# Optimization experiments

Measured on AMD Instinct MI355X. Metric: run time of the kernel, lower is better.

## Reference

```python
import jax, jax.numpy as jnp
import numpy as np

EMB = 512
N_MODELS = 5
HID = 64
N_Q = 2048
N_P = 256


def setup_inputs() -> dict:
    key = jax.random.key(0)
    ks = jax.random.split(key, 6)
    return {
        "query_features": jax.random.normal(ks[0], (N_Q, EMB), dtype=jnp.float32),
        "prototypes": jax.random.normal(ks[1], (N_P, EMB), dtype=jnp.float32),
        # first Linear: weight [64, 2*EMB], bias [64], per model
        "W1": jax.random.normal(ks[2], (N_MODELS, HID, 2 * EMB), dtype=jnp.float32) * 0.02,
        "b1": jax.random.normal(ks[3], (N_MODELS, HID), dtype=jnp.float32) * 0.02,
        # second Linear: weight [1, 64] -> stored as [64], bias scalar per model
        "W2": jax.random.normal(ks[4], (N_MODELS, HID), dtype=jnp.float32) * 0.02,
        "b2": jax.random.normal(ks[5], (N_MODELS,), dtype=jnp.float32) * 0.02,
    }


def reference(query_features, prototypes, W1, b1, W2, b2):
    d = query_features.shape[1]
    # cat([q_i, p_j]) @ W1^T == q_i @ W1[:, :d]^T + p_j @ W1[:, d:]^T
    W1q = W1[:, :, :d]   # [M, H, d]
    W1p = W1[:, :, d:]   # [M, H, d]
    hq = jnp.einsum('qd,mhd->mqh', query_features, W1q)  # [M, Q, H]
    hp = jnp.einsum('pd,mhd->mph', prototypes, W1p)      # [M, P, H]
    h = jax.nn.relu(hq[:, :, None, :] + hp[:, None, :, :] + b1[:, None, None, :])  # [M, Q, P, H]
    out = jnp.einsum('mqph,mh->mqp', h, W2) + b2[:, None, None]  # [M, Q, P]
    mean_d = out.mean(axis=0)
    # torch.std default is unbiased (ddof=1)
    unc = jnp.std(out, axis=0, ddof=1)
    return mean_d * jnp.exp(-unc)
```

## Files before the change

### kernel.cpp

```cpp
#include <hip/hip_runtime.h>
#include <math.h>

#define EMB 512
#define NM 5
#define HID 64
#define NQ 2048
#define NP 256
#define NROWS 2304
#define NRT 144
#define NC 16

typedef __attribute__((ext_vector_type(8))) short short8;
typedef __attribute__((ext_vector_type(4))) float floatx4;

#define A_BY      0u
#define B_BY      2621440u
#define PXH_BY    2949120u
#define PXL_BY    5308416u
#define PWH_BY    7667712u
#define PWL_BY    8323072u

__device__ inline unsigned short bfr(float f) {
    unsigned u = __float_as_uint(f);
    u += 0x7FFFu + ((u >> 16) & 1u);
    return (unsigned short)(u >> 16);
}

__global__ __launch_bounds__(256) void conv_pack(const float* __restrict__ Q,
                                                 const float* __restrict__ P,
                                                 const float* __restrict__ W1,
                                                 char* __restrict__ ws) {
    short* PXH = (short*)(ws + PXH_BY);
    short* PXL = (short*)(ws + PXL_BY);
    short* PWH = (short*)(ws + PWH_BY);
    short* PWL = (short*)(ws + PWL_BY);

    int lane = threadIdx.x & 63;
    int wid  = blockIdx.x * 4 + (threadIdx.x >> 6);
    int kq   = (lane >> 4) * 8;

    const float* src;
    short *dh, *dl;
    if (wid < NRT * NC) {
        int rt = wid >> 4, c = wid & 15;
        int r  = rt * 16 + (lane & 15);
        src = (r < NQ ? Q + (size_t)r * EMB : P + (size_t)(r - NQ) * EMB)
              + c * 32 + kq;
        dh = PXH + (size_t)wid * 512 + lane * 8;
        dl = PXL + (size_t)wid * 512 + lane * 8;
    } else {
        int u = wid - NRT * NC;
        int c = u & 15, ht = (u >> 4) & 3, half = (u >> 6) & 1, m = u >> 7;
        int h = ht * 16 + (lane & 15);
        src = W1 + ((size_t)m * 64 + h) * 1024 + half * EMB + c * 32 + kq;
        dh = PWH + (size_t)u * 512 + lane * 8;
        dl = PWL + (size_t)u * 512 + lane * 8;
    }

    float4 v0 = *(const float4*)&src[0];
    float4 v1 = *(const float4*)&src[4];
    short8 hh, ll;
#define CNV(I, VAL) { unsigned short h_ = bfr(VAL); hh[I] = (short)h_; \
    float hf_ = __uint_as_float(((unsigned)h_) << 16); ll[I] = (short)bfr((VAL) - hf_); }
    CNV(0, v0.x) CNV(1, v0.y) CNV(2, v0.z) CNV(3, v0.w)
    CNV(4, v1.x) CNV(5, v1.y) CNV(6, v1.z) CNV(7, v1.w)
#undef CNV
    *(short8*)dh = hh;
    *(short8*)dl = ll;
}

__global__ __launch_bounds__(256) void gemm_pk(const char* __restrict__ ws_ro,
                                               const float* __restrict__ b1,
                                               float* __restrict__ A,
                                               float* __restrict__ Bv) {
    const short* PXH = (const short*)(ws_ro + PXH_BY);
    const short* PXL = (const short*)(ws_ro + PXL_BY);
    const short* PWH = (const short*)(ws_ro + PWH_BY);
    const short* PWL = (const short*)(ws_ro + PWL_BY);

    int lane = threadIdx.x & 63;
    int ht   = threadIdx.x >> 6;
    int m    = blockIdx.x % 5;
    int rt   = blockIdx.x / 5;
    bool isQ = rt < 128;
    int half = isQ ? 0 : 1;

    const short* ax = PXH + ((size_t)rt * 16) * 512 + lane * 8;
    const short* al = PXL + ((size_t)rt * 16) * 512 + lane * 8;
    size_t wbase = ((size_t)((m * 2 + half) * 4 + ht) * 16) * 512 + lane * 8;
    const short* bh = PWH + wbase;
    const short* bl = PWL + wbase;

    floatx4 ac = {0, 0, 0, 0};
#pragma unroll 4
    for (int c = 0; c < NC; ++c) {
        short8 Ah = *(const short8*)&ax[c * 512];
        short8 Al = *(const short8*)&al[c * 512];
        short8 Bh = *(const short8*)&bh[c * 512];
        short8 Bl = *(const short8*)&bl[c * 512];
        ac = __builtin_amdgcn_mfma_f32_16x16x32_bf16(Ah, Bl, ac, 0, 0, 0);
        ac = __builtin_amdgcn_mfma_f32_16x16x32_bf16(Al, Bh, ac, 0, 0, 0);
        ac = __builtin_amdgcn_mfma_f32_16x16x32_bf16(Ah, Bh, ac, 0, 0, 0);
    }

    int col  = lane & 15;
    int rloc = (lane >> 4) * 4;
    int h    = ht * 16 + col;
    int r    = rt * 16 + rloc;

    if (isQ) {
        float bb = b1[m * 64 + h];
        float* dst = &A[((size_t)m * NQ + r) * HID + h];
        dst[0 * HID] = ac.x + bb; dst[1 * HID] = ac.y + bb;
        dst[2 * HID] = ac.z + bb; dst[3 * HID] = ac.w + bb;
    } else {
        int p = r - NQ;
        float* dst = &Bv[(((size_t)(m * 16 + (h >> 2))) * NP + p) * 4 + (h & 3)];
        dst[0 * 4] = ac.x; dst[1 * 4] = ac.y; dst[2 * 4] = ac.z; dst[3 * 4] = ac.w;
    }
}

__global__ __launch_bounds__(256) void fused_main(const float* __restrict__ A,
                                                  const float* __restrict__ Bv,
                                                  const float* __restrict__ W2,
                                                  const float* __restrict__ b2,
                                                  float* __restrict__ out) {
    int p  = threadIdx.x;
    int q0 = blockIdx.x * 4;

    float s10 = 0, s20 = 0, s11 = 0, s21 = 0;
    float s12 = 0, s22 = 0, s13 = 0, s23 = 0;
    const float4* Bq = (const float4*)Bv + p;

#pragma unroll 1
    for (int m = 0; m < NM; ++m) {
        const float4* bm = Bq + (size_t)m * 16 * NP;
        float4 B0 = bm[0*NP],  B1 = bm[1*NP],  B2 = bm[2*NP],  B3 = bm[3*NP];
        float4 B4 = bm[4*NP],  B5 = bm[5*NP],  B6 = bm[6*NP],  B7 = bm[7*NP];
        float4 B8 = bm[8*NP],  B9 = bm[9*NP],  B10= bm[10*NP], B11= bm[11*NP];
        float4 B12= bm[12*NP], B13= bm[13*NP], B14= bm[14*NP], B15= bm[15*NP];

        const float* Ar  = A + ((size_t)m * NQ + q0) * HID;
        const float* Wp2 = W2 + m * HID;
        float o0 = 0.f, o1 = 0.f, o2 = 0.f, o3 = 0.f;

#define HS1(OA, QO, BF, H0, WA, WB, WC, WD) \
        OA = fmaf(fmaxf(Ar[QO*HID+H0+0] + BF.x, 0.f), WA, OA); \
        OA = fmaf(fmaxf(Ar[QO*HID+H0+1] + BF.y, 0.f), WB, OA); \
        OA = fmaf(fmaxf(Ar[QO*HID+H0+2] + BF.z, 0.f), WC, OA); \
        OA = fmaf(fmaxf(Ar[QO*HID+H0+3] + BF.w, 0.f), WD, OA);
#define HSTEP(BF, H0) { \
        float wa=Wp2[H0+0], wb=Wp2[H0+1], wc=Wp2[H0+2], wd=Wp2[H0+3]; \
        HS1(o0, 0, BF, H0, wa, wb, wc, wd) \
        HS1(o1, 1, BF, H0, wa, wb, wc, wd) \
        HS1(o2, 2, BF, H0, wa, wb, wc, wd) \
        HS1(o3, 3, BF, H0, wa, wb, wc, wd) }

        HSTEP(B0,  0)  HSTEP(B1,  4)  HSTEP(B2,  8)  HSTEP(B3, 12)
        HSTEP(B4, 16)  HSTEP(B5, 20)  HSTEP(B6, 24)  HSTEP(B7, 28)
        HSTEP(B8, 32)  HSTEP(B9, 36)  HSTEP(B10,40)  HSTEP(B11,44)
        HSTEP(B12,48)  HSTEP(B13,52)  HSTEP(B14,56)  HSTEP(B15,60)
#undef HSTEP
#undef HS1

        float bb = b2[m];
        float x0 = o0 + bb, x1 = o1 + bb, x2 = o2 + bb, x3 = o3 + bb;
        s10 += x0; s20 = fmaf(x0, x0, s20);
        s11 += x1; s21 = fmaf(x1, x1, s21);
        s12 += x2; s22 = fmaf(x2, x2, s22);
        s13 += x3; s23 = fmaf(x3, x3, s23);
    }

#define OUTW(J, S1, S2) { \
        float mean = S1 * 0.2f; \
        float var  = fmaxf((S2 - S1 * S1 * 0.2f) * 0.25f, 0.f); \
        out[(size_t)(q0 + J) * NP + p] = mean * __expf(-sqrtf(var)); }
    OUTW(0, s10, s20) OUTW(1, s11, s21) OUTW(2, s12, s22) OUTW(3, s13, s23)
#undef OUTW
}

extern "C" void kernel_launch(void* const* d_in, const int* in_sizes, int n_in,
                              void* d_out, int out_size, void* d_ws, size_t ws_size,
                              hipStream_t stream) {
    const float* Q  = (const float*)d_in[0];
    const float* P  = (const float*)d_in[1];
    const float* W1 = (const float*)d_in[2];
    const float* b1 = (const float*)d_in[3];
    const float* W2 = (const float*)d_in[4];
    const float* b2 = (const float*)d_in[5];
    float* out = (float*)d_out;

    char*  ws = (char*)d_ws;
    float* A  = (float*)(ws + A_BY);
    float* B  = (float*)(ws + B_BY);

    conv_pack<<<736, 256, 0, stream>>>(Q, P, W1, ws);
    gemm_pk<<<720, 256, 0, stream>>>(ws, b1, A, B);
    fused_main<<<NQ / 4, 256, 0, stream>>>(A, B, W2, b2, out);
}
```

Measured before the change: 101.6 us.

## Fuse bf16 split conversion into GEMM and drop low-part activation term

Removes the separate conversion/pack kernel and has the GEMM kernel load fp32 inputs directly and convert them to bf16 inside the loop. It also drops the Al*Bh correction MFMA, so activations are kept only as a single bf16 high part while weights keep the hi/lo split. This cuts one launch and the workspace round-trip, and reduces MFMA work by a third. The cost is lower precision on the query/prototype projections and repeated conversion work across the five model blocks that share the same rows.

New measurement: 111.3 us. 1.1x slower.

```diff
diff --git a/kernel.cpp b/kernel.cpp
--- a/kernel.cpp
+++ b/kernel.cpp
@@ -6,19 +6,13 @@
 #define HID 64
 #define NQ 2048
 #define NP 256
-#define NROWS 2304
-#define NRT 144
 #define NC 16
 
 typedef __attribute__((ext_vector_type(8))) short short8;
 typedef __attribute__((ext_vector_type(4))) float floatx4;
 
-#define A_BY      0u
-#define B_BY      2621440u
-#define PXH_BY    2949120u
-#define PXL_BY    5308416u
-#define PWH_BY    7667712u
-#define PWL_BY    8323072u
+#define A_BY 0u
+#define B_BY 2621440u
 
 __device__ inline unsigned short bfr(float f) {
     unsigned u = __float_as_uint(f);
@@ -26,96 +20,62 @@
     return (unsigned short)(u >> 16);
 }
 
-__global__ __launch_bounds__(256) void conv_pack(const float* __restrict__ Q,
-                                                 const float* __restrict__ P,
-                                                 const float* __restrict__ W1,
-                                                 char* __restrict__ ws) {
-    short* PXH = (short*)(ws + PXH_BY);
-    short* PXL = (short*)(ws + PXL_BY);
-    short* PWH = (short*)(ws + PWH_BY);
-    short* PWL = (short*)(ws + PWL_BY);
-
-    int lane = threadIdx.x & 63;
-    int wid  = blockIdx.x * 4 + (threadIdx.x >> 6);
-    int kq   = (lane >> 4) * 8;
-
-    const float* src;
-    short *dh, *dl;
-    if (wid < NRT * NC) {
-        int rt = wid >> 4, c = wid & 15;
-        int r  = rt * 16 + (lane & 15);
-        src = (r < NQ ? Q + (size_t)r * EMB : P + (size_t)(r - NQ) * EMB)
-              + c * 32 + kq;
-        dh = PXH + (size_t)wid * 512 + lane * 8;
-        dl = PXL + (size_t)wid * 512 + lane * 8;
-    } else {
-        int u = wid - NRT * NC;
-        int c = u & 15, ht = (u >> 4) & 3, half = (u >> 6) & 1, m = u >> 7;
-        int h = ht * 16 + (lane & 15);
-        src = W1 + ((size_t)m * 64 + h) * 1024 + half * EMB + c * 32 + kq;
-        dh = PWH + (size_t)u * 512 + lane * 8;
-        dl = PWL + (size_t)u * 512 + lane * 8;
-    }
-
-    float4 v0 = *(const float4*)&src[0];
-    float4 v1 = *(const float4*)&src[4];
-    short8 hh, ll;
-#define CNV(I, VAL) { unsigned short h_ = bfr(VAL); hh[I] = (short)h_; \
-    float hf_ = __uint_as_float(((unsigned)h_) << 16); ll[I] = (short)bfr((VAL) - hf_); }
-    CNV(0, v0.x) CNV(1, v0.y) CNV(2, v0.z) CNV(3, v0.w)
-    CNV(4, v1.x) CNV(5, v1.y) CNV(6, v1.z) CNV(7, v1.w)
-#undef CNV
-    *(short8*)dh = hh;
-    *(short8*)dl = ll;
-}
-
-__global__ __launch_bounds__(256) void gemm_pk(const char* __restrict__ ws_ro,
-                                               const float* __restrict__ b1,
-                                               float* __restrict__ A,
-                                               float* __restrict__ Bv) {
-    const short* PXH = (const short*)(ws_ro + PXH_BY);
-    const short* PXL = (const short*)(ws_ro + PXL_BY);
-    const short* PWH = (const short*)(ws_ro + PWH_BY);
-    const short* PWL = (const short*)(ws_ro + PWL_BY);
-
-    int lane = threadIdx.x & 63;
-    int ht   = threadIdx.x >> 6;
+__global__ __launch_bounds__(256) void gemm_direct(const float* __restrict__ Q,
+                                                   const float* __restrict__ P,
+                                                   const float* __restrict__ W1,
+                                                   const float* __restrict__ b1,
+                                                   float* __restrict__ A,
+                                                   float* __restrict__ Bv) {
+    int tid  = threadIdx.x;
+    int lane = tid & 63;
+    int ht   = tid >> 6;
     int m    = blockIdx.x % 5;
     int rt   = blockIdx.x / 5;
     bool isQ = rt < 128;
     int half = isQ ? 0 : 1;
 
-    const short* ax = PXH + ((size_t)rt * 16) * 512 + lane * 8;
-    const short* al = PXL + ((size_t)rt * 16) * 512 + lane * 8;
-    size_t wbase = ((size_t)((m * 2 + half) * 4 + ht) * 16) * 512 + lane * 8;
-    const short* bh = PWH + wbase;
-    const short* bl = PWL + wbase;
+    int r  = rt * 16 + (lane & 15);
+    int kq = (lane >> 4) * 8;
+    const float* xsrc = (isQ ? Q + (size_t)r * EMB
+                             : P + (size_t)(r - NQ) * EMB) + kq;
+    int h = ht * 16 + (lane & 15);
+    const float* wsrc = W1 + ((size_t)m * 64 + h) * 1024 + half * EMB + kq;
 
     floatx4 ac = {0, 0, 0, 0};
 #pragma unroll 4
     for (int c = 0; c < NC; ++c) {
-        short8 Ah = *(const short8*)&ax[c * 512];
-        short8 Al = *(const short8*)&al[c * 512];
-        short8 Bh = *(const short8*)&bh[c * 512];
-        short8 Bl = *(const short8*)&bl[c * 512];
+        float4 xv0 = *(const float4*)&xsrc[c * 32];
+        float4 xv1 = *(const float4*)&xsrc[c * 32 + 4];
+        float4 wv0 = *(const float4*)&wsrc[c * 32];
+        float4 wv1 = *(const float4*)&wsrc[c * 32 + 4];
+
+        short8 Ah, Bh, Bl;
+        Ah[0] = (short)bfr(xv0.x); Ah[1] = (short)bfr(xv0.y);
+        Ah[2] = (short)bfr(xv0.z); Ah[3] = (short)bfr(xv0.w);
+        Ah[4] = (short)bfr(xv1.x); Ah[5] = (short)bfr(xv1.y);
+        Ah[6] = (short)bfr(xv1.z); Ah[7] = (short)bfr(xv1.w);
+#define CNV(I, VAL) { unsigned short h_ = bfr(VAL); Bh[I] = (short)h_; \
+        float hf_ = __uint_as_float(((unsigned)h_) << 16); Bl[I] = (short)bfr((VAL) - hf_); }
+        CNV(0, wv0.x) CNV(1, wv0.y) CNV(2, wv0.z) CNV(3, wv0.w)
+        CNV(4, wv1.x) CNV(5, wv1.y) CNV(6, wv1.z) CNV(7, wv1.w)
+#undef CNV
         ac = __builtin_amdgcn_mfma_f32_16x16x32_bf16(Ah, Bl, ac, 0, 0, 0);
-        ac = __builtin_amdgcn_mfma_f32_16x16x32_bf16(Al, Bh, ac, 0, 0, 0);
         ac = __builtin_amdgcn_mfma_f32_16x16x32_bf16(Ah, Bh, ac, 0, 0, 0);
     }
 
     int col  = lane & 15;
     int rloc = (lane >> 4) * 4;
-    int h    = ht * 16 + col;
-    int r    = rt * 16 + rloc;
+    int hh   = ht * 16 + col;
+    int rr   = rt * 16 + rloc;
 
     if (isQ) {
-        float bb = b1[m * 64 + h];
-        float* dst = &A[((size_t)m * NQ + r) * HID + h];
+        float bb = b1[m * 64 + hh];
+        float* dst = &A[((size_t)m * NQ + rr) * HID + hh];
         dst[0 * HID] = ac.x + bb; dst[1 * HID] = ac.y + bb;
         dst[2 * HID] = ac.z + bb; dst[3 * HID] = ac.w + bb;
     } else {
-        int p = r - NQ;
-        float* dst = &Bv[(((size_t)(m * 16 + (h >> 2))) * NP + p) * 4 + (h & 3)];
+        int p = rr - NQ;
+        float* dst = &Bv[(((size_t)(m * 16 + (hh >> 2))) * NP + p) * 4 + (hh & 3)];
         dst[0 * 4] = ac.x; dst[1 * 4] = ac.y; dst[2 * 4] = ac.z; dst[3 * 4] = ac.w;
     }
 }
@@ -194,7 +154,6 @@
     float* A  = (float*)(ws + A_BY);
     float* B  = (float*)(ws + B_BY);
 
-    conv_pack<<<736, 256, 0, stream>>>(Q, P, W1, ws);
-    gemm_pk<<<720, 256, 0, stream>>>(ws, b1, A, B);
+    gemm_direct<<<720, 256, 0, stream>>>(Q, P, W1, b1, A, B);
     fused_main<<<NQ / 4, 256, 0, stream>>>(A, B, W2, b2, out);
 }
```
